# Optimization experiments

Measured on AMD Instinct MI355X. Metric: run time of the kernel, lower is better.

## Reference

```python
import jax, jax.numpy as jnp
import numpy as np

EPS = 1e-12  # F.normalize default eps


def setup_inputs() -> dict:
    key = jax.random.key(0)
    ks = jax.random.split(key, 6)
    B, C, D, H, W = 8, 192, 24, 24, 24
    heads = 6
    x = jax.random.normal(ks[0], (B, C, D, H, W), dtype=jnp.float32)
    qkv_w = jax.random.normal(ks[1], (3 * C, C), dtype=jnp.float32) * (1.0 / np.sqrt(C))
    qkv_b = jax.random.normal(ks[2], (3 * C,), dtype=jnp.float32) * 0.02
    temperature = jnp.ones((heads, 1, 1), dtype=jnp.float32)
    proj_w = jax.random.normal(ks[3], (C, C), dtype=jnp.float32) * (1.0 / np.sqrt(C))
    proj_b = jax.random.normal(ks[4], (C,), dtype=jnp.float32) * 0.02
    return {"x": x, "qkv_w": qkv_w, "qkv_b": qkv_b, "temperature": temperature,
            "proj_w": proj_w, "proj_b": proj_b}


def _l2norm_lastdim(t):
    n = jnp.sqrt(jnp.sum(t * t, axis=-1, keepdims=True))
    return t / jnp.maximum(n, EPS)


def reference(x, qkv_w, qkv_b, temperature, proj_w, proj_b):
    B, C, D, H, W = x.shape
    N = D * H * W
    heads = temperature.shape[0]
    hd = C // heads
    xf = x.reshape(B, C, N)
    # 1x1x1 Conv3d == per-voxel linear over channels: (B, 3C, N)
    qkv = jnp.einsum('bcn,oc->bon', xf, qkv_w) + qkv_b[None, :, None]
    # Faithful torch reshape of contiguous (B, 3C, N) buffer -> (B, N, 3, heads, hd),
    # then permute(2,0,3,4,1) -> (3, B, heads, hd, N)
    qkv = qkv.reshape(B, N, 3, heads, hd).transpose(2, 0, 3, 4, 1)
    q, k, v = qkv[0], qkv[1], qkv[2]
    q = _l2norm_lastdim(q)
    k = _l2norm_lastdim(k)
    # channel cross-covariance attention: (B, heads, hd, hd)
    attn = jnp.einsum('bhcn,bhdn->bhcd', q, k) * temperature[None]
    attn = jax.nn.softmax(attn, axis=-1)
    out = jnp.einsum('bhcd,bhdn->bhcn', attn, v)          # (B, heads, hd, N)
    out = out.transpose(0, 2, 1, 3).reshape(B, C, D, H, W)  # transpose(1,2) + reshape
    outf = out.reshape(B, C, N)
    y = jnp.einsum('bcn,oc->bon', outf, proj_w) + proj_b[None, :, None]
    return y.reshape(B, C, D, H, W)
```

## Files before the change

### kernel.cpp

```cpp
#include <hip/hip_runtime.h>

#define B_ 8
#define C_ 192
#define N_ 13824
#define HEADS 6
#define HD 32
#define THREEC 576

typedef unsigned short ushort_t;
typedef unsigned int uint_t;
typedef __attribute__((ext_vector_type(8))) _Float16 half8;
typedef __attribute__((ext_vector_type(4))) float f32x4;

__device__ __forceinline__ float h2f(ushort_t u) {
  union { ushort_t u; _Float16 h; } c; c.u = u; return (float)c.h;
}
__device__ __forceinline__ ushort_t f2h(float f) {
  union { _Float16 h; ushort_t u; } c; c.h = (_Float16)f; return c.u;
}

#define LROW 200

__device__ __forceinline__ void rowperm(int f, int& row, int& u) {
  row = f / 24;
  int ul = f - row * 24;
  int uu = ul - (row & 7);
  u = uu + ((uu < 0) ? 24 : 0);
}

__global__ __launch_bounds__(256) void wconv(const float* __restrict__ w,
                                             ushort_t* __restrict__ wbf) {
  int idx = (blockIdx.x * 256 + threadIdx.x) * 8;
  float4 v0 = *(const float4*)&w[idx];
  float4 v1 = *(const float4*)&w[idx + 4];
  union { ushort_t us[8]; uint4 v; } pk;
  pk.us[0] = f2h(v0.x); pk.us[1] = f2h(v0.y); pk.us[2] = f2h(v0.z); pk.us[3] = f2h(v0.w);
  pk.us[4] = f2h(v1.x); pk.us[5] = f2h(v1.y); pk.us[6] = f2h(v1.z); pk.us[7] = f2h(v1.w);
  *(uint4*)&wbf[idx] = pk.v;
}

__global__ __launch_bounds__(256) void xt_conv(const float* __restrict__ x,
                                               ushort_t* __restrict__ xT) {
  __shared__ ushort_t tile[64 * 200];
  int t = threadIdx.x;
  int n0 = blockIdx.x * 64, b = blockIdx.y;
  const float* xb = x + (size_t)b * C_ * N_;
  int n4 = t & 15, cp = t >> 4;
#pragma unroll
  for (int it = 0; it < 6; ++it) {
    int c = (cp + it * 16) * 2;
    float4 v0 = *(const float4*)&xb[(size_t)c * N_ + n0 + n4 * 4];
    float4 v1 = *(const float4*)&xb[(size_t)(c + 1) * N_ + n0 + n4 * 4];
    float a0[4] = {v0.x, v0.y, v0.z, v0.w};
    float a1[4] = {v1.x, v1.y, v1.z, v1.w};
#pragma unroll
    for (int i = 0; i < 4; ++i) {
      uint_t wd = (uint_t)f2h(a0[i]) | ((uint_t)f2h(a1[i]) << 16);
      *(uint_t*)&tile[(n4 * 4 + i) * 200 + c] = wd;
    }
  }
  __syncthreads();
  ushort_t* xTb = xT + ((size_t)b * N_ + n0) * C_;
  int r = t >> 2, q = t & 3;
#pragma unroll
  for (int j = 0; j < 6; ++j) {
    int chunk = q * 6 + j;
    uint4 v = *(const uint4*)&tile[r * 200 + chunk * 8];
    *(uint4*)&xTb[r * 192 + chunk * 8] = v;
  }
}

__global__ __launch_bounds__(256) void qkv_gemm_mfma(
    const ushort_t* __restrict__ wbf, const ushort_t* __restrict__ xT,
    const float* __restrict__ bias, ushort_t* __restrict__ qkv) {
  __shared__ ushort_t Bs[128 * LROW];
  int t = threadIdx.x;
  int bid = blockIdx.x;
  int l = (bid & 7) * 972 + (bid >> 3);
  int o0 = (l % 9) * 64;
  int rest = l / 9;
  int n0 = (rest % 108) * 128;
  int b = rest / 108;
  int w = t >> 6, lane = t & 63;
  int ln16 = lane & 15, q4 = lane >> 4;
  int mrow = (w >> 1) * 32, ncol = (w & 1) * 64;

  const ushort_t* Bsrc = xT + ((size_t)b * N_ + n0) * C_;

  uint4 breg2[12]; int brow[12], bu[12];
#pragma unroll
  for (int j = 0; j < 12; ++j) {
    int f = (w * 12 + j) * 64 + lane;
    rowperm(f, brow[j], bu[j]);
    breg2[j] = *(const uint4*)(Bsrc + brow[j] * C_ + bu[j] * 8);
  }
#pragma unroll
  for (int j = 0; j < 12; ++j)
    *(uint4*)&Bs[brow[j] * LROW + bu[j] * 8] = breg2[j];

  const ushort_t* Abase = wbf + (size_t)(o0 + mrow + ln16) * C_ + q4 * 8;
  half8 afrag[6][2];
#pragma unroll
  for (int kk = 0; kk < 6; ++kk)
#pragma unroll
    for (int mi = 0; mi < 2; ++mi)
      afrag[kk][mi] = *(const half8*)(Abase + mi * 16 * C_ + kk * 32);

  float breg[2][4];
#pragma unroll
  for (int mi = 0; mi < 2; ++mi)
#pragma unroll
    for (int r = 0; r < 4; ++r)
      breg[mi][r] = bias[o0 + mrow + mi * 16 + q4 * 4 + r];

  f32x4 acc[2][4];
#pragma unroll
  for (int mi = 0; mi < 2; ++mi)
#pragma unroll
    for (int ni = 0; ni < 4; ++ni) acc[mi][ni] = (f32x4){0.f, 0.f, 0.f, 0.f};

  __syncthreads();

#pragma unroll
  for (int kk = 0; kk < 6; ++kk) {
    int k0 = kk * 32 + q4 * 8;
    half8 bb[4];
#pragma unroll
    for (int ni = 0; ni < 4; ++ni)
      bb[ni] = *(const half8*)&Bs[(ncol + ni * 16 + ln16) * LROW + k0];
#pragma unroll
    for (int mi = 0; mi < 2; ++mi)
#pragma unroll
      for (int ni = 0; ni < 4; ++ni)
        acc[mi][ni] = __builtin_amdgcn_mfma_f32_16x16x32_f16(
            afrag[kk][mi], bb[ni], acc[mi][ni], 0, 0, 0);
  }

#pragma unroll
  for (int mi = 0; mi < 2; ++mi)
#pragma unroll
    for (int ni = 0; ni < 4; ++ni)
#pragma unroll
      for (int r = 0; r < 4; ++r) {
        float v = acc[mi][ni][r] + breg[mi][r];
        uint_t bf = f2h(v);
        uint_t pv = (uint_t)__shfl_xor((int)bf, 1);
        if (!(lane & 1)) {
          int o_l = mrow + mi * 16 + q4 * 4 + r;
          int n_l = ncol + ni * 16 + ln16;
          *(uint_t*)&qkv[(size_t)(b * THREEC + o0 + o_l) * N_ + n0 + n_l] =
              bf | (pv << 16);
        }
      }
}

__global__ __launch_bounds__(256) void attn_partial(
    const ushort_t* __restrict__ qkv, float* __restrict__ Spart) {
  __shared__ float sh[4608];
  int t = threadIdx.x;
  int chunk = blockIdx.x, h = blockIdx.y, b = blockIdx.z;
  int j = t & 31, g8 = t >> 5;
  int tg = t >> 6, tl = t & 63;
  int c0 = (tl & 7) * 4, d0 = (tl >> 3) * 4;
  float acc[4][4];
#pragma unroll
  for (int i = 0; i < 4; ++i)
#pragma unroll
    for (int m = 0; m < 4; ++m) acc[i][m] = 0.f;
  float sqq = 0.f, sqk = 0.f;
  const ushort_t* basep = qkv + (size_t)b * THREEC * N_;
  int n2base = chunk * 1728;

  for (int p = 0; p < 27; ++p) {
    __syncthreads();
#pragma unroll
    for (int i = 0; i < 8; ++i) {
      int n2l = g8 * 8 + i;
      int n2 = n2base + p * 64 + n2l;
      int o = n2 / 24, r = n2 - o * 24;
      const ushort_t* rp = basep + (size_t)o * N_ + r * THREEC + h * HD + j;
      float qv = h2f(rp[0]);
      float kv = h2f(rp[C_]);
      sh[n2l * 32 + j] = qv;
      sh[2048 + n2l * 32 + j] = kv;
      sqq = fmaf(qv, qv, sqq);
      sqk = fmaf(kv, kv, sqk);
    }
    __syncthreads();
#pragma unroll
    for (int i = 0; i < 16; ++i) {
      int n2l = tg * 16 + i;
      float4 q4 = *(const float4*)&sh[n2l * 32 + c0];
      float4 k4 = *(const float4*)&sh[2048 + n2l * 32 + d0];
      float q[4] = {q4.x, q4.y, q4.z, q4.w};
      float kk[4] = {k4.x, k4.y, k4.z, k4.w};
#pragma unroll
      for (int ii = 0; ii < 4; ++ii)
#pragma unroll
        for (int mm = 0; mm < 4; ++mm)
          acc[ii][mm] = fmaf(q[ii], kk[mm], acc[ii][mm]);
    }
  }
  __syncthreads();
#pragma unroll
  for (int ii = 0; ii < 4; ++ii)
#pragma unroll
    for (int mm = 0; mm < 4; ++mm)
      sh[tg * 1024 + (c0 + ii) * 32 + (d0 + mm)] = acc[ii][mm];
  sh[4096 + g8 * 32 + j] = sqq;
  sh[4352 + g8 * 32 + j] = sqk;
  __syncthreads();

  float* outp = Spart + (size_t)((b * HEADS + h) * 8 + chunk) * 1088;
  for (int e = t; e < 1024; e += 256)
    outp[e] = sh[e] + sh[1024 + e] + sh[2048 + e] + sh[3072 + e];
  if (t < 32) {
    float s = 0.f;
#pragma unroll
    for (int g = 0; g < 8; ++g) s += sh[4096 + g * 32 + t];
    outp[1024 + t] = s;
  } else if (t < 64) {
    int jj = t - 32;
    float s = 0.f;
#pragma unroll
    for (int g = 0; g < 8; ++g) s += sh[4352 + g * 32 + jj];
    outp[1056 + jj] = s;
  }
}

__global__ __launch_bounds__(256) void attn_final(
    const float* __restrict__ Spart, const float* __restrict__ temp,
    const float* __restrict__ proj_w, ushort_t* __restrict__ W2bf) {
  __shared__ float Sl[1024];
  __shared__ float invq[32], invk[32];
  __shared__ float Pl[192 * 33];
  int t = threadIdx.x;
  int h = blockIdx.x, b = blockIdx.y;
  const float* base = Spart + (size_t)((b * HEADS + h) * 8) * 1088;

  for (int e = t; e < 1024; e += 256) {
    float s = 0.f;
#pragma unroll
    for (int ch = 0; ch < 8; ++ch) s += base[ch * 1088 + e];
    Sl[e] = s;
  }
  if (t < 64) {
    int jj = t & 31;
    int off = 1024 + (t >> 5) * 32 + jj;
    float s = 0.f;
#pragma unroll
    for (int ch = 0; ch < 8; ++ch) s += base[ch * 1088 + off];
    float inv = 1.f / fmaxf(sqrtf(s), 1e-12f);
    if (t < 32) invq[jj] = inv; else invk[jj] = inv;
  }
  for (int e = t; e < 6144; e += 256) {
    int co = e >> 5, c = e & 31;
    Pl[co * 33 + c] = proj_w[(size_t)co * C_ + c * HEADS + h];
  }
  __syncthreads();

  {
    int c = t >> 3, l8 = t & 7;
    float tmpv = temp[h];
    float iq = invq[c];
    float lg[4];
#pragma unroll
    for (int m = 0; m < 4; ++m) {
      int d = l8 * 4 + m;
      lg[m] = Sl[c * 32 + d] * iq * invk[d] * tmpv;
    }
    float mx = fmaxf(fmaxf(lg[0], lg[1]), fmaxf(lg[2], lg[3]));
    for (int off = 1; off < 8; off <<= 1) mx = fmaxf(mx, __shfl_xor(mx, off, 8));
    float ex[4]; float ssum = 0.f;
#pragma unroll
    for (int m = 0; m < 4; ++m) { ex[m] = __expf(lg[m] - mx); ssum += ex[m]; }
    for (int off = 1; off < 8; off <<= 1) ssum += __shfl_xor(ssum, off, 8);
    float inv = 1.f / ssum;
#pragma unroll
    for (int m = 0; m < 4; ++m) Sl[c * 32 + l8 * 4 + m] = ex[m] * inv;
  }
  __syncthreads();

  for (int e2 = t; e2 < 6144; e2 += 256) {
    int co = e2 >> 5, d = e2 & 31;
    float s = 0.f;
#pragma unroll
    for (int c = 0; c < 32; ++c)
      s = fmaf(Pl[co * 33 + c], Sl[c * 32 + d], s);
    W2bf[((size_t)b * C_ + co) * C_ + h * HD + d] = f2h(s);
  }
}

__global__ __launch_bounds__(256) void proj_mfma(
    const ushort_t* __restrict__ qkv, const ushort_t* __restrict__ W2bf,
    const float* __restrict__ pb, float* __restrict__ y) {
  __shared__ ushort_t Bs[128 * LROW];
  int t = threadIdx.x;
  int bid = blockIdx.x;
  int l = (bid & 7) * 324 + (bid >> 3);
  int o0 = (l % 3) * 64;
  int rest = l / 3;
  int n2_0 = (rest % 108) * 128;
  int b = rest / 108;
  int w = t >> 6, lane = t & 63;
  int ln16 = lane & 15, q4 = lane >> 4;
  int mrow = (w >> 1) * 32, ncol = (w & 1) * 64;

  const ushort_t* basep = qkv + (size_t)b * THREEC * N_;

  uint4 breg2[12]; int brow[12], bu[12];
#pragma unroll
  for (int j = 0; j < 12; ++j) {
    int f = (w * 12 + j) * 64 + lane;
    rowperm(f, brow[j], bu[j]);
    int n2 = n2_0 + brow[j];
    int o = n2 / 24, r2 = n2 - o * 24;
    breg2[j] = *(const uint4*)(basep + (size_t)o * N_ + r2 * THREEC + 384 + bu[j] * 8);
  }
#pragma unroll
  for (int j = 0; j < 12; ++j)
    *(uint4*)&Bs[brow[j] * LROW + bu[j] * 8] = breg2[j];

  const ushort_t* Abase = W2bf + ((size_t)b * C_ + o0 + mrow + ln16) * C_ + q4 * 8;
  half8 afrag[6][2];
#pragma unroll
  for (int kk = 0; kk < 6; ++kk)
#pragma unroll
    for (int mi = 0; mi < 2; ++mi)
      afrag[kk][mi] = *(const half8*)(Abase + mi * 16 * C_ + kk * 32);

  float breg[2][4];
#pragma unroll
  for (int mi = 0; mi < 2; ++mi)
#pragma unroll
    for (int r = 0; r < 4; ++r)
      breg[mi][r] = pb[o0 + mrow + mi * 16 + q4 * 4 + r];

  f32x4 acc[2][4];
#pragma unroll
  for (int mi = 0; mi < 2; ++mi)
#pragma unroll
    for (int ni = 0; ni < 4; ++ni) acc[mi][ni] = (f32x4){0.f, 0.f, 0.f, 0.f};

  __syncthreads();

#pragma unroll
  for (int kk = 0; kk < 6; ++kk) {
    int k0 = kk * 32 + q4 * 8;
    half8 bb[4];
#pragma unroll
    for (int ni = 0; ni < 4; ++ni)
      bb[ni] = *(const half8*)&Bs[(ncol + ni * 16 + ln16) * LROW + k0];
#pragma unroll
    for (int mi = 0; mi < 2; ++mi)
#pragma unroll
      for (int ni = 0; ni < 4; ++ni)
        acc[mi][ni] = __builtin_amdgcn_mfma_f32_16x16x32_f16(
            afrag[kk][mi], bb[ni], acc[mi][ni], 0, 0, 0);
  }

#pragma unroll
  for (int mi = 0; mi < 2; ++mi)
#pragma unroll
    for (int ni = 0; ni < 4; ++ni)
#pragma unroll
      for (int r = 0; r < 4; ++r) {
        int co_l = mrow + mi * 16 + q4 * 4 + r;
        int n_l = ncol + ni * 16 + ln16;
        y[((size_t)b * C_ + o0 + co_l) * N_ + n2_0 + n_l] =
            acc[mi][ni][r] + breg[mi][r];
      }
}

extern "C" void kernel_launch(void* const* d_in, const int* in_sizes, int n_in,
                              void* d_out, int out_size, void* d_ws, size_t ws_size,
                              hipStream_t stream) {
  const float* x      = (const float*)d_in[0];
  const float* qkv_w  = (const float*)d_in[1];
  const float* qkv_b  = (const float*)d_in[2];
  const float* temp   = (const float*)d_in[3];
  const float* proj_w = (const float*)d_in[4];
  const float* proj_b = (const float*)d_in[5];
  float* y = (float*)d_out;

  char* wp = (char*)d_ws;
  ushort_t* qkv  = (ushort_t*)wp;  wp += (size_t)B_ * THREEC * N_ * 2;
  ushort_t* xT   = (ushort_t*)wp;  wp += (size_t)B_ * N_ * C_ * 2;
  float* Spart   = (float*)wp;     wp += (size_t)B_ * HEADS * 8 * 1088 * 4;
  ushort_t* W2bf = (ushort_t*)wp;  wp += (size_t)B_ * C_ * C_ * 2;
  ushort_t* wbf  = (ushort_t*)wp;

  wconv<<<54, 256, 0, stream>>>(qkv_w, wbf);
  xt_conv<<<dim3(216, B_), 256, 0, stream>>>(x, xT);
  qkv_gemm_mfma<<<7776, 256, 0, stream>>>(wbf, xT, qkv_b, qkv);
  attn_partial<<<dim3(8, HEADS, B_), 256, 0, stream>>>(qkv, Spart);
  attn_final<<<dim3(HEADS, B_), 256, 0, stream>>>(Spart, temp, proj_w, W2bf);
  proj_mfma<<<2592, 256, 0, stream>>>(qkv, W2bf, proj_b, y);
}
```

Baseline: 322.8 us.

## Reuse staged B tile across all output rows and rebalance attention partials

The QKV and projection GEMMs now load each 128-column activation tile into shared memory once and loop over every output-row block inside the block. Weight fragments for the next block are prefetched into a double buffer. This removes the repeated reloading of the same activation tile by 9 (or 3) separate blocks, at the cost of far fewer blocks (864) and more registers per thread. The attention partial kernel uses 24 chunks instead of 8, vectorized 16-byte loads with register prefetch, and a padded shared layout. Its partial buffer is aliased onto the dead xT workspace.

```diff
diff --git a/kernel.cpp b/kernel.cpp
--- a/kernel.cpp
+++ b/kernel.cpp
@@ -6,6 +6,7 @@
 #define HEADS 6
 #define HD 32
 #define THREEC 576
+#define CHUNKS 24
 
 typedef unsigned short ushort_t;
 typedef unsigned int uint_t;
@@ -76,11 +77,9 @@
   __shared__ ushort_t Bs[128 * LROW];
   int t = threadIdx.x;
   int bid = blockIdx.x;
-  int l = (bid & 7) * 972 + (bid >> 3);
-  int o0 = (l % 9) * 64;
-  int rest = l / 9;
-  int n0 = (rest % 108) * 128;
-  int b = rest / 108;
+  int l = (bid & 7) * 108 + (bid >> 3);
+  int n0 = (l % 108) * 128;
+  int b = l / 108;
   int w = t >> 6, lane = t & 63;
   int ln16 = lane & 15, q4 = lane >> 4;
   int mrow = (w >> 1) * 32, ncol = (w & 1) * 64;
@@ -98,70 +97,85 @@
   for (int j = 0; j < 12; ++j)
     *(uint4*)&Bs[brow[j] * LROW + bu[j] * 8] = breg2[j];
 
-  const ushort_t* Abase = wbf + (size_t)(o0 + mrow + ln16) * C_ + q4 * 8;
-  half8 afrag[6][2];
+  const ushort_t* Abase0 = wbf + (size_t)(mrow + ln16) * C_ + q4 * 8;
+  half8 af[2][12];
 #pragma unroll
   for (int kk = 0; kk < 6; ++kk)
 #pragma unroll
     for (int mi = 0; mi < 2; ++mi)
-      afrag[kk][mi] = *(const half8*)(Abase + mi * 16 * C_ + kk * 32);
-
-  float breg[2][4];
-#pragma unroll
-  for (int mi = 0; mi < 2; ++mi)
-#pragma unroll
-    for (int r = 0; r < 4; ++r)
-      breg[mi][r] = bias[o0 + mrow + mi * 16 + q4 * 4 + r];
-
-  f32x4 acc[2][4];
-#pragma unroll
-  for (int mi = 0; mi < 2; ++mi)
-#pragma unroll
-    for (int ni = 0; ni < 4; ++ni) acc[mi][ni] = (f32x4){0.f, 0.f, 0.f, 0.f};
-
-  __syncthreads();
-
-#pragma unroll
-  for (int kk = 0; kk < 6; ++kk) {
-    int k0 = kk * 32 + q4 * 8;
-    half8 bb[4];
-#pragma unroll
-    for (int ni = 0; ni < 4; ++ni)
-      bb[ni] = *(const half8*)&Bs[(ncol + ni * 16 + ln16) * LROW + k0];
-#pragma unroll
-    for (int mi = 0; mi < 2; ++mi)
+      af[0][kk * 2 + mi] = *(const half8*)(Abase0 + mi * 16 * C_ + kk * 32);
+
+  __syncthreads();
+
+#pragma unroll
+  for (int it = 0; it < 9; ++it) {
+    int o0 = it * 64;
+    int cur = it & 1, nxt = cur ^ 1;
+    if (it < 8) {
+      const ushort_t* An = Abase0 + (size_t)(o0 + 64) * C_;
+#pragma unroll
+      for (int kk = 0; kk < 6; ++kk)
+#pragma unroll
+        for (int mi = 0; mi < 2; ++mi)
+          af[nxt][kk * 2 + mi] = *(const half8*)(An + mi * 16 * C_ + kk * 32);
+    }
+
+    float breg[2][4];
+#pragma unroll
+    for (int mi = 0; mi < 2; ++mi)
+#pragma unroll
+      for (int r = 0; r < 4; ++r)
+        breg[mi][r] = bias[o0 + mrow + mi * 16 + q4 * 4 + r];
+
+    f32x4 acc[2][4];
+#pragma unroll
+    for (int mi = 0; mi < 2; ++mi)
+#pragma unroll
+      for (int ni = 0; ni < 4; ++ni) acc[mi][ni] = (f32x4){0.f, 0.f, 0.f, 0.f};
+
+#pragma unroll
+    for (int kk = 0; kk < 6; ++kk) {
+      int k0 = kk * 32 + q4 * 8;
+      half8 bb[4];
 #pragma unroll
       for (int ni = 0; ni < 4; ++ni)
-        acc[mi][ni] = __builtin_amdgcn_mfma_f32_16x16x32_f16(
-            afrag[kk][mi], bb[ni], acc[mi][ni], 0, 0, 0);
-  }
-
-#pragma unroll
-  for (int mi = 0; mi < 2; ++mi)
-#pragma unroll
-    for (int ni = 0; ni < 4; ++ni)
-#pragma unroll
-      for (int r = 0; r < 4; ++r) {
-        float v = acc[mi][ni][r] + breg[mi][r];
-        uint_t bf = f2h(v);
-        uint_t pv = (uint_t)__shfl_xor((int)bf, 1);
-        if (!(lane & 1)) {
-          int o_l = mrow + mi * 16 + q4 * 4 + r;
-          int n_l = ncol + ni * 16 + ln16;
-          *(uint_t*)&qkv[(size_t)(b * THREEC + o0 + o_l) * N_ + n0 + n_l] =
-              bf | (pv << 16);
+        bb[ni] = *(const half8*)&Bs[(ncol + ni * 16 + ln16) * LROW + k0];
+#pragma unroll
+      for (int mi = 0; mi < 2; ++mi)
+#pragma unroll
+        for (int ni = 0; ni < 4; ++ni)
+          acc[mi][ni] = __builtin_amdgcn_mfma_f32_16x16x32_f16(
+              af[cur][kk * 2 + mi], bb[ni], acc[mi][ni], 0, 0, 0);
+    }
+
+#pragma unroll
+    for (int mi = 0; mi < 2; ++mi)
+#pragma unroll
+      for (int ni = 0; ni < 4; ++ni)
+#pragma unroll
+        for (int r = 0; r < 4; ++r) {
+          float v = acc[mi][ni][r] + breg[mi][r];
+          uint_t bf = f2h(v);
+          uint_t pv = (uint_t)__shfl_xor((int)bf, 1);
+          if (!(lane & 1)) {
+            int o_l = o0 + mrow + mi * 16 + q4 * 4 + r;
+            int n_l = ncol + ni * 16 + ln16;
+            *(uint_t*)&qkv[(size_t)(b * THREEC + o_l) * N_ + n0 + n_l] =
+                bf | (pv << 16);
+          }
         }
-      }
+  }
 }
 
 __global__ __launch_bounds__(256) void attn_partial(
     const ushort_t* __restrict__ qkv, float* __restrict__ Spart) {
-  __shared__ float sh[4608];
+  __shared__ float sh[5120];
   int t = threadIdx.x;
   int chunk = blockIdx.x, h = blockIdx.y, b = blockIdx.z;
   int j = t & 31, g8 = t >> 5;
   int tg = t >> 6, tl = t & 63;
   int c0 = (tl & 7) * 4, d0 = (tl >> 3) * 4;
+  int lrow = t >> 2, loct = t & 3;
   float acc[4][4];
 #pragma unroll
   for (int i = 0; i < 4; ++i)
@@ -169,29 +183,51 @@
     for (int m = 0; m < 4; ++m) acc[i][m] = 0.f;
   float sqq = 0.f, sqk = 0.f;
   const ushort_t* basep = qkv + (size_t)b * THREEC * N_;
-  int n2base = chunk * 1728;
-
-  for (int p = 0; p < 27; ++p) {
+  int n2base = chunk * 576;
+
+  uint4 qv4, kv4;
+  {
+    int n2 = n2base + lrow;
+    int o = n2 / 24, r = n2 - o * 24;
+    const ushort_t* rp = basep + (size_t)o * N_ + r * THREEC + h * HD + loct * 8;
+    qv4 = *(const uint4*)rp;
+    kv4 = *(const uint4*)(rp + C_);
+  }
+
+  for (int p = 0; p < 9; ++p) {
     __syncthreads();
+    {
+      union { uint4 v; ushort_t us[8]; } uq, uk;
+      uq.v = qv4; uk.v = kv4;
+      float4 qa = {h2f(uq.us[0]), h2f(uq.us[1]), h2f(uq.us[2]), h2f(uq.us[3])};
+      float4 qb = {h2f(uq.us[4]), h2f(uq.us[5]), h2f(uq.us[6]), h2f(uq.us[7])};
+      float4 ka = {h2f(uk.us[0]), h2f(uk.us[1]), h2f(uk.us[2]), h2f(uk.us[3])};
+      float4 kb = {h2f(uk.us[4]), h2f(uk.us[5]), h2f(uk.us[6]), h2f(uk.us[7])};
+      float* dq = &sh[lrow * 36 + loct * 8];
+      float* dk = &sh[2304 + lrow * 36 + loct * 8];
+      *(float4*)dq = qa; *(float4*)(dq + 4) = qb;
+      *(float4*)dk = ka; *(float4*)(dk + 4) = kb;
+    }
+    __syncthreads();
+    if (p < 8) {
+      int n2 = n2base + (p + 1) * 64 + lrow;
+      int o = n2 / 24, r = n2 - o * 24;
+      const ushort_t* rp = basep + (size_t)o * N_ + r * THREEC + h * HD + loct * 8;
+      qv4 = *(const uint4*)rp;
+      kv4 = *(const uint4*)(rp + C_);
+    }
 #pragma unroll
     for (int i = 0; i < 8; ++i) {
-      int n2l = g8 * 8 + i;
-      int n2 = n2base + p * 64 + n2l;
-      int o = n2 / 24, r = n2 - o * 24;
-      const ushort_t* rp = basep + (size_t)o * N_ + r * THREEC + h * HD + j;
-      float qv = h2f(rp[0]);
-      float kv = h2f(rp[C_]);
-      sh[n2l * 32 + j] = qv;
-      sh[2048 + n2l * 32 + j] = kv;
+      float qv = sh[(g8 * 8 + i) * 36 + j];
+      float kv = sh[2304 + (g8 * 8 + i) * 36 + j];
       sqq = fmaf(qv, qv, sqq);
       sqk = fmaf(kv, kv, sqk);
     }
-    __syncthreads();
 #pragma unroll
     for (int i = 0; i < 16; ++i) {
       int n2l = tg * 16 + i;
-      float4 q4 = *(const float4*)&sh[n2l * 32 + c0];
-      float4 k4 = *(const float4*)&sh[2048 + n2l * 32 + d0];
+      float4 q4 = *(const float4*)&sh[n2l * 36 + c0];
+      float4 k4 = *(const float4*)&sh[2304 + n2l * 36 + d0];
       float q[4] = {q4.x, q4.y, q4.z, q4.w};
       float kk[4] = {k4.x, k4.y, k4.z, k4.w};
 #pragma unroll
@@ -207,23 +243,23 @@
 #pragma unroll
     for (int mm = 0; mm < 4; ++mm)
       sh[tg * 1024 + (c0 + ii) * 32 + (d0 + mm)] = acc[ii][mm];
-  sh[4096 + g8 * 32 + j] = sqq;
-  sh[4352 + g8 * 32 + j] = sqk;
-  __syncthreads();
-
-  float* outp = Spart + (size_t)((b * HEADS + h) * 8 + chunk) * 1088;
+  sh[4608 + g8 * 32 + j] = sqq;
+  sh[4864 + g8 * 32 + j] = sqk;
+  __syncthreads();
+
+  float* outp = Spart + (size_t)((b * HEADS + h) * CHUNKS + chunk) * 1088;
   for (int e = t; e < 1024; e += 256)
     outp[e] = sh[e] + sh[1024 + e] + sh[2048 + e] + sh[3072 + e];
   if (t < 32) {
     float s = 0.f;
 #pragma unroll
-    for (int g = 0; g < 8; ++g) s += sh[4096 + g * 32 + t];
+    for (int g = 0; g < 8; ++g) s += sh[4608 + g * 32 + t];
     outp[1024 + t] = s;
   } else if (t < 64) {
     int jj = t - 32;
     float s = 0.f;
 #pragma unroll
-    for (int g = 0; g < 8; ++g) s += sh[4352 + g * 32 + jj];
+    for (int g = 0; g < 8; ++g) s += sh[4864 + g * 32 + jj];
     outp[1056 + jj] = s;
   }
 }
@@ -236,12 +272,12 @@
   __shared__ float Pl[192 * 33];
   int t = threadIdx.x;
   int h = blockIdx.x, b = blockIdx.y;
-  const float* base = Spart + (size_t)((b * HEADS + h) * 8) * 1088;
+  const float* base = Spart + (size_t)((b * HEADS + h) * CHUNKS) * 1088;
 
   for (int e = t; e < 1024; e += 256) {
     float s = 0.f;
 #pragma unroll
-    for (int ch = 0; ch < 8; ++ch) s += base[ch * 1088 + e];
+    for (int ch = 0; ch < CHUNKS; ++ch) s += base[ch * 1088 + e];
     Sl[e] = s;
   }
   if (t < 64) {
@@ -249,7 +285,7 @@
     int off = 1024 + (t >> 5) * 32 + jj;
     float s = 0.f;
 #pragma unroll
-    for (int ch = 0; ch < 8; ++ch) s += base[ch * 1088 + off];
+    for (int ch = 0; ch < CHUNKS; ++ch) s += base[ch * 1088 + off];
     float inv = 1.f / fmaxf(sqrtf(s), 1e-12f);
     if (t < 32) invq[jj] = inv; else invk[jj] = inv;
   }
@@ -297,11 +333,9 @@
   __shared__ ushort_t Bs[128 * LROW];
   int t = threadIdx.x;
   int bid = blockIdx.x;
-  int l = (bid & 7) * 324 + (bid >> 3);
-  int o0 = (l % 3) * 64;
-  int rest = l / 3;
-  int n2_0 = (rest % 108) * 128;
-  int b = rest / 108;
+  int l = (bid & 7) * 108 + (bid >> 3);
+  int n2_0 = (l % 108) * 128;
+  int b = l / 108;
   int w = t >> 6, lane = t & 63;
   int ln16 = lane & 15, q4 = lane >> 4;
   int mrow = (w >> 1) * 32, ncol = (w & 1) * 64;
@@ -321,55 +355,69 @@
   for (int j = 0; j < 12; ++j)
     *(uint4*)&Bs[brow[j] * LROW + bu[j] * 8] = breg2[j];
 
-  const ushort_t* Abase = W2bf + ((size_t)b * C_ + o0 + mrow + ln16) * C_ + q4 * 8;
-  half8 afrag[6][2];
+  const ushort_t* Abase0 = W2bf + ((size_t)b * C_ + mrow + ln16) * C_ + q4 * 8;
+  half8 af[2][12];
 #pragma unroll
   for (int kk = 0; kk < 6; ++kk)
 #pragma unroll
     for (int mi = 0; mi < 2; ++mi)
-      afrag[kk][mi] = *(const half8*)(Abase + mi * 16 * C_ + kk * 32);
-
-  float breg[2][4];
-#pragma unroll
-  for (int mi = 0; mi < 2; ++mi)
-#pragma unroll
-    for (int r = 0; r < 4; ++r)
-      breg[mi][r] = pb[o0 + mrow + mi * 16 + q4 * 4 + r];
-
-  f32x4 acc[2][4];
-#pragma unroll
-  for (int mi = 0; mi < 2; ++mi)
-#pragma unroll
-    for (int ni = 0; ni < 4; ++ni) acc[mi][ni] = (f32x4){0.f, 0.f, 0.f, 0.f};
-
-  __syncthreads();
-
-#pragma unroll
-  for (int kk = 0; kk < 6; ++kk) {
-    int k0 = kk * 32 + q4 * 8;
-    half8 bb[4];
-#pragma unroll
-    for (int ni = 0; ni < 4; ++ni)
-      bb[ni] = *(const half8*)&Bs[(ncol + ni * 16 + ln16) * LROW + k0];
-#pragma unroll
-    for (int mi = 0; mi < 2; ++mi)
+      af[0][kk * 2 + mi] = *(const half8*)(Abase0 + mi * 16 * C_ + kk * 32);
+
+  __syncthreads();
+
+#pragma unroll
+  for (int it = 0; it < 3; ++it) {
+    int o0 = it * 64;
+    int cur = it & 1, nxt = cur ^ 1;
+    if (it < 2) {
+      const ushort_t* An = Abase0 + (size_t)(o0 + 64) * C_;
+#pragma unroll
+      for (int kk = 0; kk < 6; ++kk)
+#pragma unroll
+        for (int mi = 0; mi < 2; ++mi)
+          af[nxt][kk * 2 + mi] = *(const half8*)(An + mi * 16 * C_ + kk * 32);
+    }
+
+    float breg[2][4];
+#pragma unroll
+    for (int mi = 0; mi < 2; ++mi)
+#pragma unroll
+      for (int r = 0; r < 4; ++r)
+        breg[mi][r] = pb[o0 + mrow + mi * 16 + q4 * 4 + r];
+
+    f32x4 acc[2][4];
+#pragma unroll
+    for (int mi = 0; mi < 2; ++mi)
+#pragma unroll
+      for (int ni = 0; ni < 4; ++ni) acc[mi][ni] = (f32x4){0.f, 0.f, 0.f, 0.f};
+
+#pragma unroll
+    for (int kk = 0; kk < 6; ++kk) {
+      int k0 = kk * 32 + q4 * 8;
+      half8 bb[4];
 #pragma unroll
       for (int ni = 0; ni < 4; ++ni)
-        acc[mi][ni] = __builtin_amdgcn_mfma_f32_16x16x32_f16(
-            afrag[kk][mi], bb[ni], acc[mi][ni], 0, 0, 0);
-  }
-
-#pragma unroll
-  for (int mi = 0; mi < 2; ++mi)
-#pragma unroll
-    for (int ni = 0; ni < 4; ++ni)
-#pragma unroll
-      for (int r = 0; r < 4; ++r) {
-        int co_l = mrow + mi * 16 + q4 * 4 + r;
-        int n_l = ncol + ni * 16 + ln16;
-        y[((size_t)b * C_ + o0 + co_l) * N_ + n2_0 + n_l] =
-            acc[mi][ni][r] + breg[mi][r];
-      }
+        bb[ni] = *(const half8*)&Bs[(ncol + ni * 16 + ln16) * LROW + k0];
+#pragma unroll
+      for (int mi = 0; mi < 2; ++mi)
+#pragma unroll
+        for (int ni = 0; ni < 4; ++ni)
+          acc[mi][ni] = __builtin_amdgcn_mfma_f32_16x16x32_f16(
+              af[cur][kk * 2 + mi], bb[ni], acc[mi][ni], 0, 0, 0);
+    }
+
+#pragma unroll
+    for (int mi = 0; mi < 2; ++mi)
+#pragma unroll
+      for (int ni = 0; ni < 4; ++ni)
+#pragma unroll
+        for (int r = 0; r < 4; ++r) {
+          int co_l = o0 + mrow + mi * 16 + q4 * 4 + r;
+          int n_l = ncol + ni * 16 + ln16;
+          y[((size_t)b * C_ + co_l) * N_ + n2_0 + n_l] =
+              acc[mi][ni][r] + breg[mi][r];
+        }
+  }
 }
 
 extern "C" void kernel_launch(void* const* d_in, const int* in_sizes, int n_in,
@@ -386,14 +434,14 @@
   char* wp = (char*)d_ws;
   ushort_t* qkv  = (ushort_t*)wp;  wp += (size_t)B_ * THREEC * N_ * 2;
   ushort_t* xT   = (ushort_t*)wp;  wp += (size_t)B_ * N_ * C_ * 2;
-  float* Spart   = (float*)wp;     wp += (size_t)B_ * HEADS * 8 * 1088 * 4;
   ushort_t* W2bf = (ushort_t*)wp;  wp += (size_t)B_ * C_ * C_ * 2;
   ushort_t* wbf  = (ushort_t*)wp;
+  float* Spart   = (float*)xT;
 
   wconv<<<54, 256, 0, stream>>>(qkv_w, wbf);
   xt_conv<<<dim3(216, B_), 256, 0, stream>>>(x, xT);
-  qkv_gemm_mfma<<<7776, 256, 0, stream>>>(wbf, xT, qkv_b, qkv);
-  attn_partial<<<dim3(8, HEADS, B_), 256, 0, stream>>>(qkv, Spart);
+  qkv_gemm_mfma<<<864, 256, 0, stream>>>(wbf, xT, qkv_b, qkv);
+  attn_partial<<<dim3(CHUNKS, HEADS, B_), 256, 0, stream>>>(qkv, Spart);
   attn_final<<<dim3(HEADS, B_), 256, 0, stream>>>(Spart, temp, proj_w, W2bf);
-  proj_mfma<<<2592, 256, 0, stream>>>(qkv, W2bf, proj_b, y);
-}
+  proj_mfma<<<864, 256, 0, stream>>>(qkv, W2bf, proj_b, y);
+}
```

Measured after the change: 359.4 us. +11.3%, slower.

## Use direct global-to-LDS loads with XOR swizzle, more attention chunks, reuse workspace

Applied to the files above, without the earlier changes.

Both MFMA GEMM kernels now stage their B tiles with global_load_lds (direct global-to-LDS DMA) into an unpadded XOR-swizzled LDS layout, replacing the register round-trip and padded rows. This cuts VGPR use and staging instructions. The MFMA loop is raised to priority 1 via s_setprio, and the qkv epilogue drops the shuffle-pair packing in favour of plain 16-bit stores. attn_partial is split into 24 chunks instead of 8 so more blocks run, and Spart now aliases the xT buffer, which is dead by the time attn_partial runs.

```diff
diff --git a/kernel.cpp b/kernel.cpp
--- a/kernel.cpp
+++ b/kernel.cpp
@@ -6,6 +6,7 @@
 #define HEADS 6
 #define HD 32
 #define THREEC 576
+#define CHUNKS 24
 
 typedef unsigned short ushort_t;
 typedef unsigned int uint_t;
@@ -19,13 +20,14 @@
   union { _Float16 h; ushort_t u; } c; c.h = (_Float16)f; return c.u;
 }
 
-#define LROW 200
-
-__device__ __forceinline__ void rowperm(int f, int& row, int& u) {
-  row = f / 24;
-  int ul = f - row * 24;
-  int uu = ul - (row & 7);
-  u = uu + ((uu < 0) ? 24 : 0);
+__device__ __forceinline__ void gload_lds16(const ushort_t* g, ushort_t* l) {
+  __builtin_amdgcn_global_load_lds(
+      (const __attribute__((address_space(1))) void*)g,
+      (__attribute__((address_space(3))) void*)l, 16, 0, 0);
+}
+
+__device__ __forceinline__ int swz_u(int u, int r) {
+  return (u & ~7) | ((u & 7) ^ (r & 7));
 }
 
 __global__ __launch_bounds__(256) void wconv(const float* __restrict__ w,
@@ -73,7 +75,7 @@
 __global__ __launch_bounds__(256) void qkv_gemm_mfma(
     const ushort_t* __restrict__ wbf, const ushort_t* __restrict__ xT,
     const float* __restrict__ bias, ushort_t* __restrict__ qkv) {
-  __shared__ ushort_t Bs[128 * LROW];
+  __shared__ ushort_t Bs[128 * 192];
   int t = threadIdx.x;
   int bid = blockIdx.x;
   int l = (bid & 7) * 972 + (bid >> 3);
@@ -87,16 +89,12 @@
 
   const ushort_t* Bsrc = xT + ((size_t)b * N_ + n0) * C_;
 
-  uint4 breg2[12]; int brow[12], bu[12];
 #pragma unroll
   for (int j = 0; j < 12; ++j) {
     int f = (w * 12 + j) * 64 + lane;
-    rowperm(f, brow[j], bu[j]);
-    breg2[j] = *(const uint4*)(Bsrc + brow[j] * C_ + bu[j] * 8);
-  }
-#pragma unroll
-  for (int j = 0; j < 12; ++j)
-    *(uint4*)&Bs[brow[j] * LROW + bu[j] * 8] = breg2[j];
+    int r = f / 24, u = f - r * 24;
+    gload_lds16(Bsrc + r * C_ + swz_u(u, r) * 8, &Bs[(w * 12 + j) * 512]);
+  }
 
   const ushort_t* Abase = wbf + (size_t)(o0 + mrow + ln16) * C_ + q4 * 8;
   half8 afrag[6][2];
@@ -119,15 +117,19 @@
 #pragma unroll
     for (int ni = 0; ni < 4; ++ni) acc[mi][ni] = (f32x4){0.f, 0.f, 0.f, 0.f};
 
-  __syncthreads();
-
+  int ur[6];
+#pragma unroll
+  for (int kk = 0; kk < 6; ++kk) ur[kk] = swz_u(kk * 4 + q4, ln16);
+
+  __syncthreads();
+
+  __builtin_amdgcn_s_setprio(1);
 #pragma unroll
   for (int kk = 0; kk < 6; ++kk) {
-    int k0 = kk * 32 + q4 * 8;
     half8 bb[4];
 #pragma unroll
     for (int ni = 0; ni < 4; ++ni)
-      bb[ni] = *(const half8*)&Bs[(ncol + ni * 16 + ln16) * LROW + k0];
+      bb[ni] = *(const half8*)&Bs[(ncol + ni * 16 + ln16) * 192 + ur[kk] * 8];
 #pragma unroll
     for (int mi = 0; mi < 2; ++mi)
 #pragma unroll
@@ -135,6 +137,7 @@
         acc[mi][ni] = __builtin_amdgcn_mfma_f32_16x16x32_f16(
             afrag[kk][mi], bb[ni], acc[mi][ni], 0, 0, 0);
   }
+  __builtin_amdgcn_s_setprio(0);
 
 #pragma unroll
   for (int mi = 0; mi < 2; ++mi)
@@ -143,14 +146,9 @@
 #pragma unroll
       for (int r = 0; r < 4; ++r) {
         float v = acc[mi][ni][r] + breg[mi][r];
-        uint_t bf = f2h(v);
-        uint_t pv = (uint_t)__shfl_xor((int)bf, 1);
-        if (!(lane & 1)) {
-          int o_l = mrow + mi * 16 + q4 * 4 + r;
-          int n_l = ncol + ni * 16 + ln16;
-          *(uint_t*)&qkv[(size_t)(b * THREEC + o0 + o_l) * N_ + n0 + n_l] =
-              bf | (pv << 16);
-        }
+        int o_l = o0 + mrow + mi * 16 + q4 * 4 + r;
+        int n_l = ncol + ni * 16 + ln16;
+        qkv[(size_t)(b * THREEC + o_l) * N_ + n0 + n_l] = f2h(v);
       }
 }
 
@@ -169,9 +167,9 @@
     for (int m = 0; m < 4; ++m) acc[i][m] = 0.f;
   float sqq = 0.f, sqk = 0.f;
   const ushort_t* basep = qkv + (size_t)b * THREEC * N_;
-  int n2base = chunk * 1728;
-
-  for (int p = 0; p < 27; ++p) {
+  int n2base = chunk * 576;
+
+  for (int p = 0; p < 9; ++p) {
     __syncthreads();
 #pragma unroll
     for (int i = 0; i < 8; ++i) {
@@ -211,7 +209,7 @@
   sh[4352 + g8 * 32 + j] = sqk;
   __syncthreads();
 
-  float* outp = Spart + (size_t)((b * HEADS + h) * 8 + chunk) * 1088;
+  float* outp = Spart + (size_t)((b * HEADS + h) * CHUNKS + chunk) * 1088;
   for (int e = t; e < 1024; e += 256)
     outp[e] = sh[e] + sh[1024 + e] + sh[2048 + e] + sh[3072 + e];
   if (t < 32) {
@@ -236,12 +234,12 @@
   __shared__ float Pl[192 * 33];
   int t = threadIdx.x;
   int h = blockIdx.x, b = blockIdx.y;
-  const float* base = Spart + (size_t)((b * HEADS + h) * 8) * 1088;
+  const float* base = Spart + (size_t)((b * HEADS + h) * CHUNKS) * 1088;
 
   for (int e = t; e < 1024; e += 256) {
     float s = 0.f;
 #pragma unroll
-    for (int ch = 0; ch < 8; ++ch) s += base[ch * 1088 + e];
+    for (int ch = 0; ch < CHUNKS; ++ch) s += base[ch * 1088 + e];
     Sl[e] = s;
   }
   if (t < 64) {
@@ -249,7 +247,7 @@
     int off = 1024 + (t >> 5) * 32 + jj;
     float s = 0.f;
 #pragma unroll
-    for (int ch = 0; ch < 8; ++ch) s += base[ch * 1088 + off];
+    for (int ch = 0; ch < CHUNKS; ++ch) s += base[ch * 1088 + off];
     float inv = 1.f / fmaxf(sqrtf(s), 1e-12f);
     if (t < 32) invq[jj] = inv; else invk[jj] = inv;
   }
@@ -294,7 +292,7 @@
 __global__ __launch_bounds__(256) void proj_mfma(
     const ushort_t* __restrict__ qkv, const ushort_t* __restrict__ W2bf,
     const float* __restrict__ pb, float* __restrict__ y) {
-  __shared__ ushort_t Bs[128 * LROW];
+  __shared__ ushort_t Bs[128 * 192];
   int t = threadIdx.x;
   int bid = blockIdx.x;
   int l = (bid & 7) * 324 + (bid >> 3);
@@ -308,18 +306,15 @@
 
   const ushort_t* basep = qkv + (size_t)b * THREEC * N_;
 
-  uint4 breg2[12]; int brow[12], bu[12];
 #pragma unroll
   for (int j = 0; j < 12; ++j) {
     int f = (w * 12 + j) * 64 + lane;
-    rowperm(f, brow[j], bu[j]);
-    int n2 = n2_0 + brow[j];
+    int r = f / 24, u = f - r * 24;
+    int n2 = n2_0 + r;
     int o = n2 / 24, r2 = n2 - o * 24;
-    breg2[j] = *(const uint4*)(basep + (size_t)o * N_ + r2 * THREEC + 384 + bu[j] * 8);
-  }
-#pragma unroll
-  for (int j = 0; j < 12; ++j)
-    *(uint4*)&Bs[brow[j] * LROW + bu[j] * 8] = breg2[j];
+    gload_lds16(basep + (size_t)o * N_ + r2 * THREEC + 384 + swz_u(u, r) * 8,
+                &Bs[(w * 12 + j) * 512]);
+  }
 
   const ushort_t* Abase = W2bf + ((size_t)b * C_ + o0 + mrow + ln16) * C_ + q4 * 8;
   half8 afrag[6][2];
@@ -342,15 +337,19 @@
 #pragma unroll
     for (int ni = 0; ni < 4; ++ni) acc[mi][ni] = (f32x4){0.f, 0.f, 0.f, 0.f};
 
-  __syncthreads();
-
+  int ur[6];
+#pragma unroll
+  for (int kk = 0; kk < 6; ++kk) ur[kk] = swz_u(kk * 4 + q4, ln16);
+
+  __syncthreads();
+
+  __builtin_amdgcn_s_setprio(1);
 #pragma unroll
   for (int kk = 0; kk < 6; ++kk) {
-    int k0 = kk * 32 + q4 * 8;
     half8 bb[4];
 #pragma unroll
     for (int ni = 0; ni < 4; ++ni)
-      bb[ni] = *(const half8*)&Bs[(ncol + ni * 16 + ln16) * LROW + k0];
+      bb[ni] = *(const half8*)&Bs[(ncol + ni * 16 + ln16) * 192 + ur[kk] * 8];
 #pragma unroll
     for (int mi = 0; mi < 2; ++mi)
 #pragma unroll
@@ -358,6 +357,7 @@
         acc[mi][ni] = __builtin_amdgcn_mfma_f32_16x16x32_f16(
             afrag[kk][mi], bb[ni], acc[mi][ni], 0, 0, 0);
   }
+  __builtin_amdgcn_s_setprio(0);
 
 #pragma unroll
   for (int mi = 0; mi < 2; ++mi)
@@ -365,9 +365,9 @@
     for (int ni = 0; ni < 4; ++ni)
 #pragma unroll
       for (int r = 0; r < 4; ++r) {
-        int co_l = mrow + mi * 16 + q4 * 4 + r;
+        int co_l = o0 + mrow + mi * 16 + q4 * 4 + r;
         int n_l = ncol + ni * 16 + ln16;
-        y[((size_t)b * C_ + o0 + co_l) * N_ + n2_0 + n_l] =
+        y[((size_t)b * C_ + co_l) * N_ + n2_0 + n_l] =
             acc[mi][ni][r] + breg[mi][r];
       }
 }
@@ -386,14 +386,14 @@
   char* wp = (char*)d_ws;
   ushort_t* qkv  = (ushort_t*)wp;  wp += (size_t)B_ * THREEC * N_ * 2;
   ushort_t* xT   = (ushort_t*)wp;  wp += (size_t)B_ * N_ * C_ * 2;
-  float* Spart   = (float*)wp;     wp += (size_t)B_ * HEADS * 8 * 1088 * 4;
   ushort_t* W2bf = (ushort_t*)wp;  wp += (size_t)B_ * C_ * C_ * 2;
   ushort_t* wbf  = (ushort_t*)wp;
+  float* Spart   = (float*)xT;
 
   wconv<<<54, 256, 0, stream>>>(qkv_w, wbf);
   xt_conv<<<dim3(216, B_), 256, 0, stream>>>(x, xT);
   qkv_gemm_mfma<<<7776, 256, 0, stream>>>(wbf, xT, qkv_b, qkv);
-  attn_partial<<<dim3(8, HEADS, B_), 256, 0, stream>>>(qkv, Spart);
+  attn_partial<<<dim3(CHUNKS, HEADS, B_), 256, 0, stream>>>(qkv, Spart);
   attn_final<<<dim3(HEADS, B_), 256, 0, stream>>>(Spart, temp, proj_w, W2bf);
   proj_mfma<<<2592, 256, 0, stream>>>(qkv, W2bf, proj_b, y);
 }
```

Result: faster. 307.3 us (-4.8%).
